# Kernel tuning notes

Measured on AMD Instinct MI355X. Metric: run time of the kernel, lower is better.

The kernel has to match this reference:

```python
import jax, jax.numpy as jnp
import numpy as np

HID = 400
K = 10  # attention mixture components


def _lstm_cell(x, h, c, Wih, Whh, b):
    # torch gate order: i, f, g, o
    g = x @ Wih.T + h @ Whh.T + b
    i, f, gg, o = jnp.split(g, 4, axis=-1)
    c = jax.nn.sigmoid(f) * c + jax.nn.sigmoid(i) * jnp.tanh(gg)
    h = jax.nn.sigmoid(o) * jnp.tanh(c)
    return h, c


def setup_inputs() -> dict:
    key = jax.random.key(0)
    ks = jax.random.split(key, 14)
    B, T, U, D = 64, 600, 64, 60
    s = 0.08  # keep exp() in attention numerically tame
    strokes = jax.random.normal(ks[0], (B, T, 3), dtype=jnp.float32)
    ids = jax.random.randint(ks[1], (B, U), 0, D)
    onehots = jax.nn.one_hot(ids, D, dtype=jnp.float32)
    text_mask = jnp.ones((B, U), dtype=jnp.float32)
    W_ih1 = jax.random.normal(ks[2], (4 * HID, D + 3)) * s
    W_hh1 = jax.random.normal(ks[3], (4 * HID, HID)) * s
    b1 = jax.random.normal(ks[4], (4 * HID,)) * s  # b_ih + b_hh combined
    W_win = jax.random.normal(ks[5], (3 * K, HID)) * s
    b_win = jax.random.normal(ks[6], (3 * K,)) * s
    W_ih2 = jax.random.normal(ks[7], (4 * HID, 3 + D + HID)) * s
    W_hh2 = jax.random.normal(ks[8], (4 * HID, HID)) * s
    b2 = jax.random.normal(ks[9], (4 * HID,)) * s
    W_fc = jax.random.normal(ks[10], (121, 2 * HID)) * s
    b_fc = jax.random.normal(ks[11], (121,)) * s
    return {"strokes": strokes, "onehots": onehots, "text_mask": text_mask,
            "W_ih1": W_ih1, "W_hh1": W_hh1, "b1": b1,
            "W_win": W_win, "b_win": b_win,
            "W_ih2": W_ih2, "W_hh2": W_hh2, "b2": b2,
            "W_fc": W_fc, "b_fc": b_fc}


def reference(strokes, onehots, text_mask, W_ih1, W_hh1, b1, W_win, b_win,
              W_ih2, W_hh2, b2, W_fc, b_fc):
    B, T, _ = strokes.shape
    U = onehots.shape[1]
    u = jnp.arange(U, dtype=jnp.float32)

    def step1(carry, x_t):
        h0, c0, kappa, w = carry
        h0, c0 = _lstm_cell(jnp.concatenate([x_t, w], -1), h0, c0, W_ih1, W_hh1, b1)
        p = jnp.exp(h0 @ W_win.T + b_win)              # [B, 3K]
        alpha, beta, kap = jnp.split(p, 3, axis=-1)    # each [B, K]
        kappa = kappa + kap
        diff = kappa[:, None, :] - u[None, :, None]    # [B, U, K]
        phi = jnp.sum(alpha[:, None, :] * jnp.exp(-beta[:, None, :] * diff * diff), -1)
        phi = phi * text_mask                          # [B, U]
        w = jnp.einsum('bu,bud->bd', phi, onehots)     # [B, D]
        return (h0, c0, kappa, w), (h0, w, phi)

    z = jnp.zeros((B, HID), jnp.float32)
    init = (z, z, jnp.zeros((B, K), jnp.float32), onehots[:, 0, :])
    (h0f, c0f, kappa_f, w_f), (H1, Wt, Phi) = jax.lax.scan(step1, init, strokes.transpose(1, 0, 2))
    lstm1_out = H1.transpose(1, 0, 2)                  # [B, T, 400]
    attn_out = Wt.transpose(1, 0, 2)                   # [B, T, D]
    phi_last = Phi[-1]

    x2 = jnp.concatenate([strokes, attn_out, lstm1_out], -1)  # [B, T, 463]

    def step2(carry, x_t):
        h, c = carry
        h, c = _lstm_cell(x_t, h, c, W_ih2, W_hh2, b2)
        return (h, c), h

    (h1f, c1f), H2 = jax.lax.scan(step2, (z, z), x2.transpose(1, 0, 2))
    lstm2_out = H2.transpose(1, 0, 2)                  # [B, T, 400]

    out = jnp.concatenate([lstm1_out, lstm2_out], -1) @ W_fc.T + b_fc  # [B, T, 121]
    mu, log_sigma, pi, rho, eos = jnp.split(out, [40, 80, 100, 120], axis=-1)
    rho = jnp.tanh(rho)
    pi = jax.nn.softmax(pi, axis=-1)
    eos = jax.nn.sigmoid(-eos)
    mu = mu.reshape(B, T, 20, 2)
    sigma = log_sigma.reshape(B, T, 20, 2)  # original returns raw log-sigma reshaped
    return (pi, mu, sigma, rho, eos, w_f, kappa_f, phi_last, h0f, c0f, h1f, c1f)
```

## Files before the change

### kernel.cpp

```cpp
#include <hip/hip_runtime.h>
#include <hip/hip_bf16.h>
#include <math.h>

#define HIDN 400
#define KK   10
#define UU   64
#define DD   60
#define TT   600
#define FCIN 800
#define FCOUT 121

#define NH1  100
#define NH2  100
#define NWBK 16
#define WBAT 4
#define TOTB 216
#define THR  1024
#define NWAVE 16
#define CB   16
#define PSTR 68

#define SLOT1 25600
#define SLOTW 3840

#define PI_OFF    0
#define MU_OFF    768000
#define SIG_OFF   2304000
#define RHO_OFF   3840000
#define EOS_OFF   4608000
#define WF_OFF    4646400
#define KAPPA_OFF 4650240
#define PHI_OFF   4650880
#define H0F_OFF   4654976
#define C0F_OFF   4680576
#define H1F_OFF   4706176
#define C1F_OFF   4731776

#define WS_H1T   0
#define WS_H2T   15385600
#define WS_WHT   30771200
#define WS_XST   33079040
#define WS_WALL1 33194240
#define WS_WALL2 33935040
#define WS_WFCT  35315840
#define WS_CNT   35412640

#define CAI(i,g) ((((i)&7)*13+(g))*16)
#define CWI(i,g) (1664 + (((i)&7)*2+(g))*16)
#define CHI(i,g) (1920 + (((i)&7)*13+(g))*16)
#define CNT_INTS 3584
#define TGT8(i)  ((((i)>>3)+1)*8)
#define TGT4(i)  ((((i)>>3)+1)*4)

#define SMEM_F 32512

__device__ __forceinline__ float sigm(float x){ return 1.0f/(1.0f + expf(-x)); }

__device__ __forceinline__ void st_agent(float* p, float v){
  __hip_atomic_store(p, v, __ATOMIC_RELAXED, __HIP_MEMORY_SCOPE_AGENT);
}
__device__ __forceinline__ int ld_agent_i(const int* p){
  return __hip_atomic_load(p, __ATOMIC_RELAXED, __HIP_MEMORY_SCOPE_AGENT);
}
__device__ __forceinline__ void arrive(int* p){
  __hip_atomic_fetch_add(p, 1, __ATOMIC_RELAXED, __HIP_MEMORY_SCOPE_AGENT);
}
__device__ __forceinline__ void spin_ge(const int* w, int tgt){
  if (ld_agent_i(w) >= tgt) return;
  do { __builtin_amdgcn_s_sleep(1); } while (ld_agent_i(w) < tgt);
}

__global__ void prep_init(const float* __restrict__ onehots, const float* __restrict__ strokes,
                          float* __restrict__ H1t, float* __restrict__ H2t,
                          float* __restrict__ Wh,  float* __restrict__ XST,
                          int* __restrict__ cnts){
  int idx = blockIdx.x*blockDim.x + threadIdx.x;
  if (idx < SLOT1){ H1t[idx] = 0.f; H2t[idx] = 0.f; }
  if (idx < SLOTW){
    int d = idx >> 6, b = idx & 63;
    Wh[idx] = onehots[b*(UU*DD) + d];
  }
  if (idx < TT*3*64){
    int t = idx/192, rem = idx%192, comp = rem/64, b = rem%64;
    XST[idx] = strokes[(b*TT + t)*3 + comp];
  }
  if (idx < CNT_INTS) cnts[idx] = 0;
}

__global__ void prep_wall(const float* __restrict__ Wih1, const float* __restrict__ Whh1,
                          const float* __restrict__ Wih2, const float* __restrict__ Whh2,
                          float* __restrict__ WALL1, float* __restrict__ WALL2){
  int idx = blockIdx.x*blockDim.x + threadIdx.x;
  if (idx < 640000){
    int g = idx/400, k = idx%400;
    int q = g/400, j = g%400, pp = j>>2, c = 4*q + (j&3);
    WALL1[((size_t)pp*463 + k)*CB + c] = Whh1[idx];
  } else if (idx < 740800){
    int s = idx - 640000;
    int g = s/63, col = s%63;
    int q = g/400, j = g%400, pp = j>>2, c = 4*q + (j&3);
    int r = (col < 3) ? (460 + col) : (400 + col - 3);
    WALL1[((size_t)pp*463 + r)*CB + c] = Wih1[s];
  } else if (idx < 1380800){
    int s = idx - 740800;
    int g = s/400, k = s%400;
    int q = g/400, j = g%400, pp = j>>2, c = 4*q + (j&3);
    WALL2[((size_t)pp*863 + 400 + k)*CB + c] = Whh2[s];
  } else if (idx < 2121600){
    int s = idx - 1380800;
    int g = s/463, col = s%463;
    int q = g/400, j = g%400, pp = j>>2, c = 4*q + (j&3);
    int r = (col<3) ? (860+col) : (col<63 ? (800+col-3) : (col-63));
    WALL2[((size_t)pp*863 + r)*CB + c] = Wih2[s];
  }
}

__global__ void prep_wfc(const float* __restrict__ Wfc, float* __restrict__ WfcT){
  int idx = blockIdx.x*blockDim.x + threadIdx.x;
  if (idx >= FCIN*FCOUT) return;
  int k = idx / FCOUT, j = idx - k*FCOUT;
  WfcT[idx] = Wfc[j*FCIN + k];
}

__device__ __forceinline__ void gemv16(const float* __restrict__ x,
                                       const float* __restrict__ w,
                                       int n, int bg4, int cg4, float acc[16]){
  #pragma unroll 4
  for (int k=0;k<n;++k){
    const float4 xv = *(const float4*)(x + k*64 + bg4);
    const float4 wv = *(const float4*)(w + k*CB + cg4);
    acc[0]  = fmaf(wv.x, xv.x, acc[0]);
    acc[1]  = fmaf(wv.x, xv.y, acc[1]);
    acc[2]  = fmaf(wv.x, xv.z, acc[2]);
    acc[3]  = fmaf(wv.x, xv.w, acc[3]);
    acc[4]  = fmaf(wv.y, xv.x, acc[4]);
    acc[5]  = fmaf(wv.y, xv.y, acc[5]);
    acc[6]  = fmaf(wv.y, xv.z, acc[6]);
    acc[7]  = fmaf(wv.y, xv.w, acc[7]);
    acc[8]  = fmaf(wv.z, xv.x, acc[8]);
    acc[9]  = fmaf(wv.z, xv.y, acc[9]);
    acc[10] = fmaf(wv.z, xv.z, acc[10]);
    acc[11] = fmaf(wv.z, xv.w, acc[11]);
    acc[12] = fmaf(wv.w, xv.x, acc[12]);
    acc[13] = fmaf(wv.w, xv.y, acc[13]);
    acc[14] = fmaf(wv.w, xv.z, acc[14]);
    acc[15] = fmaf(wv.w, xv.w, acc[15]);
  }
}

__global__ __launch_bounds__(THR) void recurrent_kernel(
    const float* __restrict__ Wwin, const float* __restrict__ bwin,
    const float* __restrict__ b1g,  const float* __restrict__ b2g,
    const float* __restrict__ tmask,const float* __restrict__ onehots,
    const float* __restrict__ WALL1,const float* __restrict__ WALL2,
    float* __restrict__ H1t,        float* __restrict__ H2t,
    float* __restrict__ Wh,         const float* __restrict__ XST,
    int* __restrict__ cnts,         float* __restrict__ outp)
{
  const int p   = blockIdx.x;
  const int tid = threadIdx.x;
  __shared__ float SM[SMEM_F];

  if (p < NH1){
    const int wave = tid >> 6, lane = tid & 63;
    const int bg4  = (lane & 15) * 4;
    const int cg4  = (lane >> 4) * 4;
    float* WL1 = SM;          float* PART = SM + 7408;
    float* GRED= SM + 24816;  float* CS   = SM + 25840;
    float* BS  = SM + 26096;

    for (int idx = tid; idx < 463*CB; idx += THR) WL1[idx] = WALL1[(size_t)p*463*CB + idx];
    if (tid < 16){ int q = tid>>2, u = tid&3; BS[tid] = b1g[q*HIDN + 4*p + u]; }
    if (tid < 256) CS[tid] = 0.f;
    __syncthreads();

    for (int i = 0; i < TT; ++i){
      float acc[16];
      #pragma unroll
      for (int z=0; z<16; ++z) acc[z] = 0.f;
      const int k0 = wave*26, k1 = min(k0 + 26, 403);
      if (i >= 1){
        int kh = min(k1, 400);
        if (kh > k0){
          int g0 = k0 >> 5, g1 = (kh-1) >> 5;
          for (int g = g0; g <= g1; ++g)
            spin_ge(&cnts[CAI(i-1,g)], (g==12) ? TGT4(i-1) : TGT8(i-1));
          asm volatile("" ::: "memory");
        }
      }
      {
        const float* __restrict__ H1prev = H1t + (size_t)i*SLOT1;
        { int ka = k0, kb = min(k1, 400);
          if (kb > ka) gemv16(H1prev + ka*64, WL1 + ka*CB, kb-ka, bg4, cg4, acc); }
        { int ka = max(k0,400), kb = k1;
          if (kb > ka) gemv16(XST + i*192 + (ka-400)*64, WL1 + (460+(ka-400))*CB, kb-ka, bg4, cg4, acc); }
      }
      if (i >= 1){
        spin_ge(&cnts[CWI(i-1,0)], TGT8(i-1));
        spin_ge(&cnts[CWI(i-1,1)], TGT8(i-1));
        asm volatile("" ::: "memory");
      }
      {
        const float* __restrict__ Whp = Wh + (size_t)i*SLOTW;
        int m0 = wave*4, m1 = min(m0 + 4, 60);
        if (m1 > m0) gemv16(Whp + m0*64, WL1 + (400+m0)*CB, m1-m0, bg4, cg4, acc);
      }
      #pragma unroll
      for (int cc=0; cc<4; ++cc)
        *(float4*)&PART[(wave*16 + cg4 + cc)*PSTR + bg4] =
          make_float4(acc[cc*4+0], acc[cc*4+1], acc[cc*4+2], acc[cc*4+3]);
      __syncthreads();
      {
        int c = tid>>6, b = tid&63; float s = 0.f;
        #pragma unroll
        for (int w16=0; w16<NWAVE; ++w16) s += PART[(w16*16 + c)*PSTR + b];
        GRED[c*64 + b] = s;
      }
      __syncthreads();
      if (tid < 256){
        int u = tid>>6, b = tid&63, j = 4*p + u;
        float gi = GRED[( 0+u)*64+b] + BS[ 0+u];
        float gf = GRED[( 4+u)*64+b] + BS[ 4+u];
        float gg = GRED[( 8+u)*64+b] + BS[ 8+u];
        float go = GRED[(12+u)*64+b] + BS[12+u];
        float c_ = sigm(gf)*CS[u*64+b] + sigm(gi)*tanhf(gg);
        float h_ = sigm(go)*tanhf(c_);
        CS[u*64+b] = c_;
        st_agent(&H1t[(size_t)(i+1)*SLOT1 + j*64 + b], h_);
        if (i == TT-1){ outp[H0F_OFF + b*HIDN + j] = h_; outp[C0F_OFF + b*HIDN + j] = c_; }
      }
      __syncthreads();
      if (tid == 0) arrive(&cnts[CAI(i, p>>3)]);
    }
  } else if (p < NH1 + NH2){
    const int q2 = p - NH1;
    const int wave = tid >> 6, lane = tid & 63;
    const int bg4  = (lane & 15) * 4;
    const int cg4  = (lane >> 4) * 4;
    float* WL2 = SM;          float* PART = SM + 13808;
    float* GRED= SM + 31216;  float* CS   = SM + 32240;
    float* BS  = SM + 32496;

    for (int idx = tid; idx < 863*CB; idx += THR) WL2[idx] = WALL2[(size_t)q2*863*CB + idx];
    if (tid < 16){ int q = tid>>2, u = tid&3; BS[tid] = b2g[q*HIDN + 4*q2 + u]; }
    if (tid < 256) CS[tid] = 0.f;
    __syncthreads();

    for (int t2 = 0; t2 < TT; ++t2){
      float acc[16];
      #pragma unroll
      for (int z=0; z<16; ++z) acc[z] = 0.f;
      spin_ge(&cnts[CWI(t2,0)], TGT8(t2));
      spin_ge(&cnts[CWI(t2,1)], TGT8(t2));
      asm volatile("" ::: "memory");
      {
        const float* __restrict__ H1v = H1t + (size_t)(t2+1)*SLOT1;
        const float* __restrict__ Whv = Wh  + (size_t)(t2+1)*SLOTW;
        int k0 = wave*29, k1 = min(k0 + 29, 463);
        { int ka = k0, kb = min(k1, 400);
          if (kb > ka) gemv16(H1v + ka*64, WL2 + ka*CB, kb-ka, bg4, cg4, acc); }
        { int ka = max(k0,400), kb = min(k1, 460);
          if (kb > ka) gemv16(Whv + (ka-400)*64, WL2 + (800+(ka-400))*CB, kb-ka, bg4, cg4, acc); }
        { int ka = max(k0,460), kb = k1;
          if (kb > ka) gemv16(XST + t2*192 + (ka-460)*64, WL2 + (860+(ka-460))*CB, kb-ka, bg4, cg4, acc); }
      }
      const int m0 = wave*25, m1 = min(m0 + 25, 400);
      if (t2 >= 1 && m1 > m0){
        int g0 = m0 >> 5, g1 = (m1-1) >> 5;
        for (int g = g0; g <= g1; ++g)
          spin_ge(&cnts[CHI(t2-1,g)], (g==12) ? TGT4(t2-1) : TGT8(t2-1));
        asm volatile("" ::: "memory");
      }
      {
        const float* __restrict__ H2v = H2t + (size_t)t2*SLOT1;
        if (m1 > m0) gemv16(H2v + m0*64, WL2 + (400+m0)*CB, m1-m0, bg4, cg4, acc);
      }
      #pragma unroll
      for (int cc=0; cc<4; ++cc)
        *(float4*)&PART[(wave*16 + cg4 + cc)*PSTR + bg4] =
          make_float4(acc[cc*4+0], acc[cc*4+1], acc[cc*4+2], acc[cc*4+3]);
      __syncthreads();
      {
        int c = tid>>6, b = tid&63; float s = 0.f;
        #pragma unroll
        for (int w16=0; w16<NWAVE; ++w16) s += PART[(w16*16 + c)*PSTR + b];
        GRED[c*64 + b] = s;
      }
      __syncthreads();
      if (tid < 256){
        int u = tid>>6, b = tid&63, j = 4*q2 + u;
        float gi = GRED[( 0+u)*64+b] + BS[ 0+u];
        float gf = GRED[( 4+u)*64+b] + BS[ 4+u];
        float gg = GRED[( 8+u)*64+b] + BS[ 8+u];
        float go = GRED[(12+u)*64+b] + BS[12+u];
        float c_ = sigm(gf)*CS[u*64+b] + sigm(gi)*tanhf(gg);
        float h_ = sigm(go)*tanhf(c_);
        CS[u*64+b] = c_;
        st_agent(&H2t[(size_t)(t2+1)*SLOT1 + j*64 + b], h_);
        if (t2 == TT-1){ outp[H1F_OFF + b*HIDN + j] = h_; outp[C1F_OFF + b*HIDN + j] = c_; }
      }
      __syncthreads();
      if (tid == 0) arrive(&cnts[CHI(t2, q2>>3)]);
    }
  } else {
    const int wb = p - NH1 - NH2;
    const int b0 = wb * WBAT;
    const int wave = tid >> 6, lane = tid & 63;
    float* WWT = SM;          float* ONE = SM + 13200;
    float* H1S = SM + 28848;  float* TMS = SM + 30848;
    float* PW  = SM + 31104;  float* KAP = SM + 31232;
    float* PHI = SM + 31296;  float* BWS = SM + 31552;

    for (int idx = tid; idx < 30*400; idx += THR){
      int j = idx/400, k = idx - j*400;
      WWT[k*33 + j] = Wwin[idx];
    }
    for (int idx = tid; idx < WBAT*UU*DD; idx += THR){
      int b = idx/3840, rem = idx - b*3840, u = rem/60, d = rem - u*60;
      ONE[b*3912 + u*61 + d] = onehots[(size_t)(b0+b)*3840 + rem];
    }
    if (tid < WBAT*UU) TMS[tid] = tmask[b0*UU + tid];
    if (tid < WBAT*16) KAP[tid] = 0.f;
    if (tid < 30) BWS[tid] = bwin[tid];
    __syncthreads();

    for (int i = 0; i < TT; ++i){
      const float* __restrict__ H1now = H1t + (size_t)(i+1)*SLOT1;
      if (wave < 13){
        spin_ge(&cnts[CAI(i,wave)], (wave==12) ? TGT4(i) : TGT8(i));
        asm volatile("" ::: "memory");
        const int nrows = (wave==12) ? 16 : 32;
        const int base  = wave*32;
        for (int idx = lane; idx < nrows*WBAT; idx += 64){
          int k = base + (idx >> 2), bb = idx & 3;
          H1S[k*5 + bb] = H1now[k*64 + b0 + bb];
        }
      }
      __syncthreads();
      if (tid < 960){
        int ks = tid & 7, pair = tid >> 3;
        int b = pair / 30, j = pair - b*30;
        float s = 0.f;
        #pragma unroll
        for (int kk = 0; kk < 50; ++kk){
          int k = ks*50 + kk;
          s = fmaf(H1S[k*5 + b], WWT[k*33 + j], s);
        }
        s += __shfl_down(s, 4, 8);
        s += __shfl_down(s, 2, 8);
        s += __shfl_down(s, 1, 8);
        if (ks == 0) PW[b*32 + j] = expf(s + BWS[j]);
      }
      __syncthreads();
      if (tid < WBAT*KK){
        int b = tid/KK, k = tid - b*KK;
        KAP[b*16 + k] += PW[b*32 + 20 + k];
      }
      __syncthreads();
      if (tid < WBAT*UU){
        int b = tid >> 6, u = tid & 63;
        float uf = (float)u, s = 0.f;
        #pragma unroll
        for (int q = 0; q < KK; ++q){
          float d = KAP[b*16 + q] - uf;
          s = fmaf(PW[b*32 + q], expf(-PW[b*32 + 10 + q]*d*d), s);
        }
        s *= TMS[b*64 + u];
        PHI[b*64 + u] = s;
        if (i == TT-1) outp[PHI_OFF + (b0+b)*UU + u] = s;
      }
      __syncthreads();
      if (tid < WBAT*DD){
        int d = tid >> 2, b = tid & 3;
        float s = 0.f;
        #pragma unroll 8
        for (int u = 0; u < UU; ++u) s = fmaf(PHI[b*64 + u], ONE[b*3912 + u*61 + d], s);
        st_agent(&Wh[(size_t)(i+1)*SLOTW + d*64 + b0 + b], s);
        if (i == TT-1) outp[WF_OFF + (b0+b)*DD + d] = s;
      }
      if (i == TT-1 && tid < WBAT*KK){
        int b = tid/KK, k = tid - b*KK;
        outp[KAPPA_OFF + (b0+b)*KK + k] = KAP[b*16 + k];
      }
      __syncthreads();
      if (tid == 0) arrive(&cnts[CWI(i, wb>>3)]);
    }
  }
}

__global__ __launch_bounds__(128) void fc2_kernel(
    const float* __restrict__ H1t, const float* __restrict__ H2t,
    const float* __restrict__ WfcT, const float* __restrict__ bfc,
    float* __restrict__ outp)
{
  const int t   = blockIdx.x;
  const int tid = threadIdx.x;
  __shared__ float Xs[8][64];
  __shared__ float OUT[FCOUT][65];
  float acc[64];
  #pragma unroll
  for (int b=0;b<64;++b) acc[b]=0.f;
  const float* __restrict__ base1 = H1t + (size_t)(t+1)*SLOT1;
  const float* __restrict__ base2 = H2t + (size_t)(t+1)*SLOT1;

  for (int kb=0; kb<100; ++kb){
    __syncthreads();
    #pragma unroll
    for (int e=0;e<4;++e){
      int idx = e*128 + tid;
      int row = idx>>6, b = idx&63;
      int k = kb*8 + row;
      Xs[row][b] = (k<400) ? base1[k*64+b] : base2[(k-400)*64+b];
    }
    __syncthreads();
    if (tid < FCOUT){
      #pragma unroll
      for (int kk=0;kk<8;++kk){
        float wv = WfcT[(kb*8+kk)*FCOUT + tid];
        #pragma unroll
        for (int b4=0;b4<16;++b4){
          float4 xv = *(const float4*)&Xs[kk][b4*4];
          acc[b4*4+0] = fmaf(wv, xv.x, acc[b4*4+0]);
          acc[b4*4+1] = fmaf(wv, xv.y, acc[b4*4+1]);
          acc[b4*4+2] = fmaf(wv, xv.z, acc[b4*4+2]);
          acc[b4*4+3] = fmaf(wv, xv.w, acc[b4*4+3]);
        }
      }
    }
  }
  if (tid < FCOUT){
    float bj = bfc[tid];
    #pragma unroll
    for (int b=0;b<64;++b) OUT[tid][b] = acc[b] + bj;
  }
  __syncthreads();
  if (tid < 64){
    const int b = tid;
    const size_t pos = (size_t)b*TT + t;
    for (int j=0;j<40;++j) outp[MU_OFF  + pos*40 + j] = OUT[j][b];
    for (int j=0;j<40;++j) outp[SIG_OFF + pos*40 + j] = OUT[40+j][b];
    float m = -1e30f;
    for (int q=0;q<20;++q) m = fmaxf(m, OUT[80+q][b]);
    float e[20], s=0.f;
    for (int q=0;q<20;++q){ e[q]=expf(OUT[80+q][b]-m); s+=e[q]; }
    float inv = 1.f/s;
    for (int q=0;q<20;++q) outp[PI_OFF  + pos*20 + q] = e[q]*inv;
    for (int q=0;q<20;++q) outp[RHO_OFF + pos*20 + q] = tanhf(OUT[100+q][b]);
    outp[EOS_OFF + pos] = 1.0f/(1.0f + expf(OUT[120][b]));
  }
}

extern "C" void kernel_launch(void* const* d_in, const int* in_sizes, int n_in,
                              void* d_out, int out_size, void* d_ws, size_t ws_size,
                              hipStream_t stream){
  (void)in_sizes; (void)n_in; (void)out_size; (void)ws_size;
  const float* strokes = (const float*)d_in[0];
  const float* onehots = (const float*)d_in[1];
  const float* tmask   = (const float*)d_in[2];
  const float* Wih1    = (const float*)d_in[3];
  const float* Whh1    = (const float*)d_in[4];
  const float* b1      = (const float*)d_in[5];
  const float* Wwin    = (const float*)d_in[6];
  const float* bwin    = (const float*)d_in[7];
  const float* Wih2    = (const float*)d_in[8];
  const float* Whh2    = (const float*)d_in[9];
  const float* b2      = (const float*)d_in[10];
  const float* Wfc     = (const float*)d_in[11];
  const float* bfc     = (const float*)d_in[12];

  float* ws    = (float*)d_ws;
  float* outp  = (float*)d_out;
  float* H1t   = ws + WS_H1T;
  float* H2t   = ws + WS_H2T;
  float* Wh    = ws + WS_WHT;
  float* XST   = ws + WS_XST;
  float* WALL1 = ws + WS_WALL1;
  float* WALL2 = ws + WS_WALL2;
  float* WfcT  = ws + WS_WFCT;
  int*   cnts  = (int*)(ws + WS_CNT);

  hipLaunchKernelGGL(prep_init, dim3((TT*3*64 + 255)/256), dim3(256), 0, stream,
                     onehots, strokes, H1t, H2t, Wh, XST, cnts);
  hipLaunchKernelGGL(prep_wall, dim3((2121600 + 255)/256), dim3(256), 0, stream,
                     Wih1, Whh1, Wih2, Whh2, WALL1, WALL2);
  hipLaunchKernelGGL(prep_wfc, dim3((FCIN*FCOUT + 255)/256), dim3(256), 0, stream,
                     Wfc, WfcT);

  hipLaunchKernelGGL(recurrent_kernel, dim3(TOTB), dim3(THR), 0, stream,
                     Wwin, bwin, b1, b2, tmask, onehots, WALL1, WALL2,
                     H1t, H2t, Wh, XST, cnts, outp);

  hipLaunchKernelGGL(fc2_kernel, dim3(TT), dim3(128), 0, stream,
                     H1t, H2t, WfcT, bfc, outp);
}
```

Before: 7.727 ms.

## Compute attention window redundantly inside each LSTM1 block, dropping window blocks

Removes the 16 dedicated attention-window blocks. Every LSTM1 block now computes the full window itself: the gemv against W_win, the exps, the kappa update, phi, and the window vector for all 64 batches, kept in shared memory. The one-hot matmul is replaced by a scatter-add using character indices precomputed in the prep kernel. The aim is to remove one cross-block handoff per timestep from the critical recurrence path. In exchange, each block does redundant work with a 400-long serial dot-product loop reading global H1, and waits on all 13 H1 groups each step. LSTM2 now syncs on a single counter published by block 0.

```diff
diff --git a/kernel.cpp b/kernel.cpp
--- a/kernel.cpp
+++ b/kernel.cpp
@@ -12,9 +12,7 @@
 
 #define NH1  100
 #define NH2  100
-#define NWBK 16
-#define WBAT 4
-#define TOTB 216
+#define TOTB 200
 #define THR  1024
 #define NWAVE 16
 #define CB   16
@@ -44,19 +42,23 @@
 #define WS_WALL2 33935040
 #define WS_WFCT  35315840
 #define WS_CNT   35412640
+#define WS_IDS   35415984
 
 #define CAI(i,g) ((((i)&7)*13+(g))*16)
-#define CWI(i,g) (1664 + (((i)&7)*2+(g))*16)
-#define CHI(i,g) (1920 + (((i)&7)*13+(g))*16)
-#define CNT_INTS 3584
+#define CHI(i,g) (1664 + (((i)&7)*13+(g))*16)
+#define CWW_IDX  3328
+#define CNT_INTS 3344
 #define TGT8(i)  ((((i)>>3)+1)*8)
 #define TGT4(i)  ((((i)>>3)+1)*4)
 
-#define SMEM_F 32512
+#define SMEM_F 40512
 
 __device__ __forceinline__ float sigm(float x){ return 1.0f/(1.0f + expf(-x)); }
 
 __device__ __forceinline__ void st_agent(float* p, float v){
+  __hip_atomic_store(p, v, __ATOMIC_RELAXED, __HIP_MEMORY_SCOPE_AGENT);
+}
+__device__ __forceinline__ void st_agent_i(int* p, int v){
   __hip_atomic_store(p, v, __ATOMIC_RELAXED, __HIP_MEMORY_SCOPE_AGENT);
 }
 __device__ __forceinline__ int ld_agent_i(const int* p){
@@ -73,7 +75,7 @@
 __global__ void prep_init(const float* __restrict__ onehots, const float* __restrict__ strokes,
                           float* __restrict__ H1t, float* __restrict__ H2t,
                           float* __restrict__ Wh,  float* __restrict__ XST,
-                          int* __restrict__ cnts){
+                          int* __restrict__ cnts,  int* __restrict__ ids){
   int idx = blockIdx.x*blockDim.x + threadIdx.x;
   if (idx < SLOT1){ H1t[idx] = 0.f; H2t[idx] = 0.f; }
   if (idx < SLOTW){
@@ -85,6 +87,13 @@
     XST[idx] = strokes[(b*TT + t)*3 + comp];
   }
   if (idx < CNT_INTS) cnts[idx] = 0;
+  if (idx < 4096){
+    int b = idx >> 6, u = idx & 63;
+    const float* oh = onehots + (size_t)(b*UU + u)*DD;
+    int d = 0;
+    for (int q = 0; q < DD; ++q) if (oh[q] > 0.5f) d = q;
+    ids[idx] = d;
+  }
 }
 
 __global__ void prep_wall(const float* __restrict__ Wih1, const float* __restrict__ Whh1,
@@ -151,7 +160,7 @@
 __global__ __launch_bounds__(THR) void recurrent_kernel(
     const float* __restrict__ Wwin, const float* __restrict__ bwin,
     const float* __restrict__ b1g,  const float* __restrict__ b2g,
-    const float* __restrict__ tmask,const float* __restrict__ onehots,
+    const float* __restrict__ tmask,const int* __restrict__ ids_g,
     const float* __restrict__ WALL1,const float* __restrict__ WALL2,
     float* __restrict__ H1t,        float* __restrict__ H2t,
     float* __restrict__ Wh,         const float* __restrict__ XST,
@@ -165,74 +174,168 @@
     const int wave = tid >> 6, lane = tid & 63;
     const int bg4  = (lane & 15) * 4;
     const int cg4  = (lane >> 4) * 4;
-    float* WL1 = SM;          float* PART = SM + 7408;
-    float* GRED= SM + 24816;  float* CS   = SM + 25840;
-    float* BS  = SM + 26096;
+    float* WL1 = SM;
+    float* WWT = SM + 7408;
+    float* PART= SM + 19408;
+    float* GRED= SM + 28112;
+    float* WLOC= SM + 29136;
+    float* PW  = SM + 32976;
+    float* KAP = SM + 35024;
+    float* PHT = SM + 36048;
+    float* CS  = SM + 40208;
+    float* BS  = SM + 40464;
+    float* BWS = SM + 40480;
 
     for (int idx = tid; idx < 463*CB; idx += THR) WL1[idx] = WALL1[(size_t)p*463*CB + idx];
+    for (int idx = tid; idx < 30*400; idx += THR){
+      int j = idx/400, k = idx - j*400;
+      WWT[k*30 + j] = Wwin[idx];
+    }
     if (tid < 16){ int q = tid>>2, u = tid&3; BS[tid] = b1g[q*HIDN + 4*p + u]; }
     if (tid < 256) CS[tid] = 0.f;
+    if (tid < 1024 && tid < 64*16) KAP[tid] = 0.f;
+    if (tid < 30) BWS[tid] = bwin[tid];
     __syncthreads();
 
-    for (int i = 0; i < TT; ++i){
+    for (int i = 0; i <= TT; ++i){
+      if (i == TT && p != 0) break;
       float acc[16];
       #pragma unroll
       for (int z=0; z<16; ++z) acc[z] = 0.f;
       const int k0 = wave*26, k1 = min(k0 + 26, 403);
-      if (i >= 1){
-        int kh = min(k1, 400);
-        if (kh > k0){
-          int g0 = k0 >> 5, g1 = (kh-1) >> 5;
-          for (int g = g0; g <= g1; ++g)
-            spin_ge(&cnts[CAI(i-1,g)], (g==12) ? TGT4(i-1) : TGT8(i-1));
-          asm volatile("" ::: "memory");
-        }
-      }
-      {
+
+      if (i < TT){
+        if (i >= 1){
+          int kh = min(k1, 400);
+          if (kh > k0){
+            int g0 = k0 >> 5, g1 = (kh-1) >> 5;
+            for (int g = g0; g <= g1; ++g)
+              spin_ge(&cnts[CAI(i-1,g)], (g==12) ? TGT4(i-1) : TGT8(i-1));
+            asm volatile("" ::: "memory");
+          }
+        }
         const float* __restrict__ H1prev = H1t + (size_t)i*SLOT1;
         { int ka = k0, kb = min(k1, 400);
           if (kb > ka) gemv16(H1prev + ka*64, WL1 + ka*CB, kb-ka, bg4, cg4, acc); }
         { int ka = max(k0,400), kb = k1;
           if (kb > ka) gemv16(XST + i*192 + (ka-400)*64, WL1 + (460+(ka-400))*CB, kb-ka, bg4, cg4, acc); }
       }
+
       if (i >= 1){
-        spin_ge(&cnts[CWI(i-1,0)], TGT8(i-1));
-        spin_ge(&cnts[CWI(i-1,1)], TGT8(i-1));
+        if (tid < 13) spin_ge(&cnts[CAI(i-1,tid)], (tid==12) ? TGT4(i-1) : TGT8(i-1));
         asm volatile("" ::: "memory");
       }
-      {
-        const float* __restrict__ Whp = Wh + (size_t)i*SLOTW;
-        int m0 = wave*4, m1 = min(m0 + 4, 60);
-        if (m1 > m0) gemv16(Whp + m0*64, WL1 + (400+m0)*CB, m1-m0, bg4, cg4, acc);
-      }
-      #pragma unroll
-      for (int cc=0; cc<4; ++cc)
-        *(float4*)&PART[(wave*16 + cg4 + cc)*PSTR + bg4] =
-          make_float4(acc[cc*4+0], acc[cc*4+1], acc[cc*4+2], acc[cc*4+3]);
-      __syncthreads();
-      {
-        int c = tid>>6, b = tid&63; float s = 0.f;
+      __syncthreads();
+
+      if (i == 0){
+        for (int idx = tid; idx < 3840; idx += THR) WLOC[idx] = Wh[idx];
+      } else {
+        for (int idx = tid; idx < 3840; idx += THR) WLOC[idx] = 0.f;
+        const float* __restrict__ H1prev = H1t + (size_t)i*SLOT1;
+        if (tid < 960){
+          int b = tid/15, jj = tid - (tid/15)*15;
+          float s0 = 0.f, s1 = 0.f;
+          #pragma unroll 4
+          for (int k = 0; k < 400; ++k){
+            float hv = H1prev[k*64 + b];
+            s0 = fmaf(hv, WWT[k*30 + jj],      s0);
+            s1 = fmaf(hv, WWT[k*30 + jj + 15], s1);
+          }
+          PW[b*32 + jj]      = expf(s0 + BWS[jj]);
+          PW[b*32 + jj + 15] = expf(s1 + BWS[jj + 15]);
+        }
+      }
+      __syncthreads();
+      if (i >= 1){
+        if (tid < 640){ int b = tid/10, q = tid - (tid/10)*10; KAP[b*16+q] += PW[b*32+20+q]; }
+      }
+      __syncthreads();
+      if (i >= 1){
         #pragma unroll
-        for (int w16=0; w16<NWAVE; ++w16) s += PART[(w16*16 + c)*PSTR + b];
-        GRED[c*64 + b] = s;
-      }
-      __syncthreads();
-      if (tid < 256){
-        int u = tid>>6, b = tid&63, j = 4*p + u;
-        float gi = GRED[( 0+u)*64+b] + BS[ 0+u];
-        float gf = GRED[( 4+u)*64+b] + BS[ 4+u];
-        float gg = GRED[( 8+u)*64+b] + BS[ 8+u];
-        float go = GRED[(12+u)*64+b] + BS[12+u];
-        float c_ = sigm(gf)*CS[u*64+b] + sigm(gi)*tanhf(gg);
-        float h_ = sigm(go)*tanhf(c_);
-        CS[u*64+b] = c_;
-        st_agent(&H1t[(size_t)(i+1)*SLOT1 + j*64 + b], h_);
-        if (i == TT-1){ outp[H0F_OFF + b*HIDN + j] = h_; outp[C0F_OFF + b*HIDN + j] = c_; }
-      }
-      __syncthreads();
-      if (tid == 0) arrive(&cnts[CAI(i, p>>3)]);
+        for (int it = 0; it < 4; ++it){
+          int pair = it*1024 + tid;
+          int b = pair >> 6, u = pair & 63;
+          float uf = (float)u, s = 0.f;
+          #pragma unroll
+          for (int q = 0; q < KK; ++q){
+            float d = KAP[b*16+q] - uf;
+            s = fmaf(PW[b*32+q], expf(-PW[b*32+10+q]*d*d), s);
+          }
+          s *= tmask[b*64 + u];
+          PHT[u*65 + b] = s;
+          if (i == TT && p == 0) outp[PHI_OFF + b*64 + u] = s;
+        }
+      }
+      __syncthreads();
+      if (i >= 1){
+        #pragma unroll
+        for (int it = 0; it < 4; ++it){
+          int pair = it*1024 + tid;
+          int u = pair >> 6, b = pair & 63;
+          float v = PHT[u*65 + b];
+          int d = ids_g[b*64 + u];
+          atomicAdd(&WLOC[d*64 + b], v);
+        }
+      }
+      __syncthreads();
+      if (p == 0 && i >= 1){
+        for (int idx = tid; idx < 3840; idx += THR)
+          st_agent(&Wh[(size_t)i*SLOTW + idx], WLOC[idx]);
+      }
+
+      if (i < TT){
+        { int m0 = wave*4, m1 = min(m0 + 4, 60);
+          if (m1 > m0) gemv16(WLOC + m0*64, WL1 + (400+m0)*CB, m1-m0, bg4, cg4, acc); }
+        if (wave < 8){
+          #pragma unroll
+          for (int cc=0; cc<4; ++cc)
+            *(float4*)&PART[(wave*16 + cg4 + cc)*PSTR + bg4] =
+              make_float4(acc[cc*4+0], acc[cc*4+1], acc[cc*4+2], acc[cc*4+3]);
+        }
+        __syncthreads();
+        if (wave >= 8){
+          #pragma unroll
+          for (int cc=0; cc<4; ++cc){
+            float4* p4 = (float4*)&PART[((wave-8)*16 + cg4 + cc)*PSTR + bg4];
+            float4 v = *p4;
+            v.x += acc[cc*4+0]; v.y += acc[cc*4+1]; v.z += acc[cc*4+2]; v.w += acc[cc*4+3];
+            *p4 = v;
+          }
+        }
+        __syncthreads();
+        {
+          int c = tid >> 6, b = tid & 63; float s = 0.f;
+          #pragma unroll
+          for (int w8 = 0; w8 < 8; ++w8) s += PART[(w8*16 + c)*PSTR + b];
+          GRED[c*64 + b] = s;
+        }
+        __syncthreads();
+        if (tid < 256){
+          int u = tid>>6, b = tid&63, j = 4*p + u;
+          float gi = GRED[( 0+u)*64+b] + BS[ 0+u];
+          float gf = GRED[( 4+u)*64+b] + BS[ 4+u];
+          float gg = GRED[( 8+u)*64+b] + BS[ 8+u];
+          float go = GRED[(12+u)*64+b] + BS[12+u];
+          float c_ = sigm(gf)*CS[u*64+b] + sigm(gi)*tanhf(gg);
+          float h_ = sigm(go)*tanhf(c_);
+          CS[u*64+b] = c_;
+          st_agent(&H1t[(size_t)(i+1)*SLOT1 + j*64 + b], h_);
+          if (i == TT-1){ outp[H0F_OFF + b*HIDN + j] = h_; outp[C0F_OFF + b*HIDN + j] = c_; }
+        }
+        __syncthreads();
+        if (tid == 0) arrive(&cnts[CAI(i, p>>3)]);
+        if (p == 0 && tid == 64) st_agent_i(&cnts[CWW_IDX], i);
+      } else {
+        __syncthreads();
+        if (tid == 0) st_agent_i(&cnts[CWW_IDX], TT);
+        for (int idx = tid; idx < 3840; idx += THR){
+          int d = idx >> 6, b = idx & 63;
+          outp[WF_OFF + b*DD + d] = WLOC[idx];
+        }
+        if (tid < 640){ int b = tid/10, q = tid - (tid/10)*10; outp[KAPPA_OFF + b*KK + q] = KAP[b*16+q]; }
+      }
     }
-  } else if (p < NH1 + NH2){
+  } else {
     const int q2 = p - NH1;
     const int wave = tid >> 6, lane = tid & 63;
     const int bg4  = (lane & 15) * 4;
@@ -250,9 +353,9 @@
       float acc[16];
       #pragma unroll
       for (int z=0; z<16; ++z) acc[z] = 0.f;
-      spin_ge(&cnts[CWI(t2,0)], TGT8(t2));
-      spin_ge(&cnts[CWI(t2,1)], TGT8(t2));
+      if (tid == 0) spin_ge(&cnts[CWW_IDX], t2+1);
       asm volatile("" ::: "memory");
+      __syncthreads();
       {
         const float* __restrict__ H1v = H1t + (size_t)(t2+1)*SLOT1;
         const float* __restrict__ Whv = Wh  + (size_t)(t2+1)*SLOTW;
@@ -301,89 +404,6 @@
       }
       __syncthreads();
       if (tid == 0) arrive(&cnts[CHI(t2, q2>>3)]);
-    }
-  } else {
-    const int wb = p - NH1 - NH2;
-    const int b0 = wb * WBAT;
-    const int wave = tid >> 6, lane = tid & 63;
-    float* WWT = SM;          float* ONE = SM + 13200;
-    float* H1S = SM + 28848;  float* TMS = SM + 30848;
-    float* PW  = SM + 31104;  float* KAP = SM + 31232;
-    float* PHI = SM + 31296;  float* BWS = SM + 31552;
-
-    for (int idx = tid; idx < 30*400; idx += THR){
-      int j = idx/400, k = idx - j*400;
-      WWT[k*33 + j] = Wwin[idx];
-    }
-    for (int idx = tid; idx < WBAT*UU*DD; idx += THR){
-      int b = idx/3840, rem = idx - b*3840, u = rem/60, d = rem - u*60;
-      ONE[b*3912 + u*61 + d] = onehots[(size_t)(b0+b)*3840 + rem];
-    }
-    if (tid < WBAT*UU) TMS[tid] = tmask[b0*UU + tid];
-    if (tid < WBAT*16) KAP[tid] = 0.f;
-    if (tid < 30) BWS[tid] = bwin[tid];
-    __syncthreads();
-
-    for (int i = 0; i < TT; ++i){
-      const float* __restrict__ H1now = H1t + (size_t)(i+1)*SLOT1;
-      if (wave < 13){
-        spin_ge(&cnts[CAI(i,wave)], (wave==12) ? TGT4(i) : TGT8(i));
-        asm volatile("" ::: "memory");
-        const int nrows = (wave==12) ? 16 : 32;
-        const int base  = wave*32;
-        for (int idx = lane; idx < nrows*WBAT; idx += 64){
-          int k = base + (idx >> 2), bb = idx & 3;
-          H1S[k*5 + bb] = H1now[k*64 + b0 + bb];
-        }
-      }
-      __syncthreads();
-      if (tid < 960){
-        int ks = tid & 7, pair = tid >> 3;
-        int b = pair / 30, j = pair - b*30;
-        float s = 0.f;
-        #pragma unroll
-        for (int kk = 0; kk < 50; ++kk){
-          int k = ks*50 + kk;
-          s = fmaf(H1S[k*5 + b], WWT[k*33 + j], s);
-        }
-        s += __shfl_down(s, 4, 8);
-        s += __shfl_down(s, 2, 8);
-        s += __shfl_down(s, 1, 8);
-        if (ks == 0) PW[b*32 + j] = expf(s + BWS[j]);
-      }
-      __syncthreads();
-      if (tid < WBAT*KK){
-        int b = tid/KK, k = tid - b*KK;
-        KAP[b*16 + k] += PW[b*32 + 20 + k];
-      }
-      __syncthreads();
-      if (tid < WBAT*UU){
-        int b = tid >> 6, u = tid & 63;
-        float uf = (float)u, s = 0.f;
-        #pragma unroll
-        for (int q = 0; q < KK; ++q){
-          float d = KAP[b*16 + q] - uf;
-          s = fmaf(PW[b*32 + q], expf(-PW[b*32 + 10 + q]*d*d), s);
-        }
-        s *= TMS[b*64 + u];
-        PHI[b*64 + u] = s;
-        if (i == TT-1) outp[PHI_OFF + (b0+b)*UU + u] = s;
-      }
-      __syncthreads();
-      if (tid < WBAT*DD){
-        int d = tid >> 2, b = tid & 3;
-        float s = 0.f;
-        #pragma unroll 8
-        for (int u = 0; u < UU; ++u) s = fmaf(PHI[b*64 + u], ONE[b*3912 + u*61 + d], s);
-        st_agent(&Wh[(size_t)(i+1)*SLOTW + d*64 + b0 + b], s);
-        if (i == TT-1) outp[WF_OFF + (b0+b)*DD + d] = s;
-      }
-      if (i == TT-1 && tid < WBAT*KK){
-        int b = tid/KK, k = tid - b*KK;
-        outp[KAPPA_OFF + (b0+b)*KK + k] = KAP[b*16 + k];
-      }
-      __syncthreads();
-      if (tid == 0) arrive(&cnts[CWI(i, wb>>3)]);
     }
   }
 }
@@ -478,16 +498,17 @@
   float* WALL2 = ws + WS_WALL2;
   float* WfcT  = ws + WS_WFCT;
   int*   cnts  = (int*)(ws + WS_CNT);
+  int*   ids   = (int*)(ws + WS_IDS);
 
   hipLaunchKernelGGL(prep_init, dim3((TT*3*64 + 255)/256), dim3(256), 0, stream,
-                     onehots, strokes, H1t, H2t, Wh, XST, cnts);
+                     onehots, strokes, H1t, H2t, Wh, XST, cnts, ids);
   hipLaunchKernelGGL(prep_wall, dim3((2121600 + 255)/256), dim3(256), 0, stream,
                      Wih1, Whh1, Wih2, Whh2, WALL1, WALL2);
   hipLaunchKernelGGL(prep_wfc, dim3((FCIN*FCOUT + 255)/256), dim3(256), 0, stream,
                      Wfc, WfcT);
 
   hipLaunchKernelGGL(recurrent_kernel, dim3(TOTB), dim3(THR), 0, stream,
-                     Wwin, bwin, b1, b2, tmask, onehots, WALL1, WALL2,
+                     Wwin, bwin, b1, b2, tmask, ids, WALL1, WALL2,
                      H1t, H2t, Wh, XST, cnts, outp);
 
   hipLaunchKernelGGL(fc2_kernel, dim3(TT), dim3(128), 0, stream,
```

Result: slower. 17.08 ms (+121.1%).
